# Performance work log

Measured on AMD Instinct MI355X. Metric: run time of the kernel, lower is better.

The kernel has to match this reference:

```python
import jax, jax.numpy as jnp
import numpy as np


def _conv1x1(x, W, b):
    # x: [B,C,H,W] (NCHW), W: [out,in] (1x1 conv kernel), b: [out]
    return jnp.einsum('bchw,oc->bohw', x, W) + b[None, :, None, None]


def setup_inputs() -> dict:
    key = jax.random.key(0)
    ks = jax.random.split(key, 12)
    B, C, H, W = 8, 256, 64, 64
    s = 1.0 / np.sqrt(C)
    x = jax.random.normal(ks[0], (B, C, H, W), dtype=jnp.float32)
    mask = jnp.round(jax.random.uniform(ks[1], (B, 1, H, W), dtype=jnp.float32))
    Wq = jax.random.normal(ks[2], (C, C), dtype=jnp.float32) * s
    bq = jax.random.normal(ks[3], (C,), dtype=jnp.float32) * 0.01
    Wk = jax.random.normal(ks[4], (C, C), dtype=jnp.float32) * s
    bk = jax.random.normal(ks[5], (C,), dtype=jnp.float32) * 0.01
    Wv = jax.random.normal(ks[6], (C, C), dtype=jnp.float32) * s
    bv = jax.random.normal(ks[7], (C,), dtype=jnp.float32) * 0.01
    Wo = jax.random.normal(ks[8], (C, C), dtype=jnp.float32) * s
    bo = jax.random.normal(ks[9], (C,), dtype=jnp.float32) * 0.01
    gamma = jnp.zeros((1,), dtype=jnp.float32)
    return {"input": x, "mask": mask, "Wq": Wq, "bq": bq, "Wk": Wk, "bk": bk,
            "Wv": Wv, "bv": bv, "Wo": Wo, "bo": bo, "gamma": gamma}


def reference(input, mask, Wq, bq, Wk, bk, Wv, bv, Wo, bo, gamma):
    B, C, H, W = input.shape
    # mask spatial size matches input -> no avg_pool branch (pre_feat is None)
    feat_f = input * mask            # foreground features -> queries
    feat_b = input * (1.0 - mask)    # background features -> keys/values
    q = _conv1x1(feat_f, Wq, bq).reshape(B, C, -1)   # [B,C,N]
    k = _conv1x1(feat_b, Wk, bk).reshape(B, C, -1)   # [B,C,N]
    v = _conv1x1(feat_b, Wv, bv).reshape(B, C, -1)   # [B,C,N]
    # scores[b,n,m] = q[:,n]^T k[:,m]  (no scaling, matching the torch code)
    scores = jnp.einsum('bcn,bcm->bnm', q, k)        # [B,N,N]
    attn = jax.nn.softmax(scores, axis=-1)
    out = jnp.einsum('bnm,bcm->bcn', attn, v).reshape(B, C, H, W)
    out = _conv1x1(out, Wo, bo)
    return out + gamma * input
```

## Files before the change

kernel.cpp:

```cpp
#include <hip/hip_runtime.h>

#define CC 256
#define NN 4096
#define NB 8
#define NM ((size_t)CC * NN)

typedef _Float16 f16;
typedef f16 f16x4 __attribute__((ext_vector_type(4)));
typedef f16 f16x8 __attribute__((ext_vector_type(8)));
typedef float f32x4 __attribute__((ext_vector_type(4)));
typedef unsigned int u32;

#define GLD16(gp, lp) __builtin_amdgcn_global_load_lds( \
    (const __attribute__((address_space(1))) u32*)(const void*)(gp), \
    (__attribute__((address_space(3))) u32*)(void*)(lp), 16, 0, 0)

__global__ __launch_bounds__(256) void mask_scan_kernel(
    const float* __restrict__ mask, int* __restrict__ posm, int* __restrict__ counts)
{
    const int b = blockIdx.x;
    const int t = threadIdx.x;
    const int lane = t & 63, w = t >> 6;
    __shared__ int wsum[4];
    const float* mp = mask + (size_t)b * NN;
    int* pp = posm + (size_t)b * NN;

    int loc[16], cnt = 0;
#pragma unroll
    for (int i = 0; i < 16; ++i) {
        loc[i] = cnt;
        cnt += (mp[t * 16 + i] == 0.0f) ? 1 : 0;
    }
    int inc = cnt;
#pragma unroll
    for (int d = 1; d < 64; d <<= 1) {
        int v = __shfl_up(inc, d, 64);
        if (lane >= d) inc += v;
    }
    if (lane == 63) wsum[w] = inc;
    int exc = inc - cnt;
    __syncthreads();
    int base = exc;
    for (int i = 0; i < w; ++i) base += wsum[i];
#pragma unroll
    for (int i = 0; i < 16; ++i)
        pp[t * 16 + i] = (mp[t * 16 + i] == 0.0f) ? (base + loc[i]) : -1;
    if (t == 0) counts[b] = wsum[0] + wsum[1] + wsum[2] + wsum[3];
}

__global__ __launch_bounds__(256, 2) void proj_fused_kernel(
    const float* __restrict__ x, const float* __restrict__ mask,
    const float* __restrict__ Wq, const float* __restrict__ bq,
    const float* __restrict__ Wk, const float* __restrict__ bk,
    const float* __restrict__ Wv, const float* __restrict__ bv,
    f16* __restrict__ wsh, const int* __restrict__ posm,
    const int* __restrict__ counts, int b0)
{
    __shared__ f16x8 xf[2048];
    __shared__ f16x8 xb[2048];

    const int t = threadIdx.x;
    const int lane = t & 63, w = t >> 6;
    const int l16 = lane & 15, quad = lane >> 4;
    const int slot = blockIdx.x;
    const int b = b0 + slot;
    const int n0 = blockIdx.y * 64;
    const float* xp = x + (size_t)b * NM;
    f16* base = wsh + (size_t)slot * 4 * NM;
    const int* pom = posm + (size_t)b * NN;

    float mf  = mask[(size_t)b * NN + n0 + lane];
    float mbk = 1.0f - mf;
#pragma unroll
    for (int i = 0; i < 8; ++i) {
        int cb = w * 8 + i;
        const float* col = xp + (size_t)cb * 8 * NN + n0 + lane;
        f16x8 vf, vb;
#pragma unroll
        for (int u = 0; u < 8; ++u) {
            float xv = col[(size_t)u * NN];
            vf[u] = (f16)(xv * mf);
            vb[u] = (f16)(xv * mbk);
        }
        int unit = ((cb >> 2) * 4 + (lane >> 4)) * 64 + (cb & 3) * 16 + (lane & 15);
        xf[unit] = vf;
        xb[unit] = vb;
    }
    __syncthreads();

#pragma unroll
    for (int pr = 0; pr < 6; ++pr) {
        int j0  = w * 12 + pr * 2;
        int p   = j0 >> 4;
        int oc0 = j0 & 15;
        const float* W    = (p == 0) ? Wq : (p == 1) ? Wk : Wv;
        const float* bias = (p == 0) ? bq : (p == 1) ? bk : bv;
        const f16x8* bt   = (p == 0) ? xf : xb;

        f16x8 wf[2][8];
#pragma unroll
        for (int h = 0; h < 2; ++h) {
            const float* wrow = W + (size_t)((oc0 + h) * 16 + l16) * CC + quad * 8;
#pragma unroll
            for (int kc = 0; kc < 8; ++kc) {
                float4 a = *(const float4*)(wrow + kc * 32);
                float4 c = *(const float4*)(wrow + kc * 32 + 4);
                f16x8 f;
                f[0] = (f16)a.x; f[1] = (f16)a.y; f[2] = (f16)a.z; f[3] = (f16)a.w;
                f[4] = (f16)c.x; f[5] = (f16)c.y; f[6] = (f16)c.z; f[7] = (f16)c.w;
                wf[h][kc] = f;
            }
        }
        f32x4 acc[2][4];
#pragma unroll
        for (int h = 0; h < 2; ++h)
#pragma unroll
            for (int nc = 0; nc < 4; ++nc) acc[h][nc] = (f32x4){0.f, 0.f, 0.f, 0.f};
#pragma unroll
        for (int nc = 0; nc < 4; ++nc)
#pragma unroll
            for (int kc = 0; kc < 8; ++kc) {
                f16x8 bf = bt[(kc * 4 + nc) * 64 + lane];
                acc[0][nc] = __builtin_amdgcn_mfma_f32_16x16x32_f16(wf[0][kc], bf, acc[0][nc], 0, 0, 0);
                acc[1][nc] = __builtin_amdgcn_mfma_f32_16x16x32_f16(wf[1][kc], bf, acc[1][nc], 0, 0, 0);
            }
#pragma unroll
        for (int h = 0; h < 2; ++h) {
            int oc = oc0 + h;
            float bvv[4];
#pragma unroll
            for (int r = 0; r < 4; ++r) bvv[r] = bias[oc * 16 + quad * 4 + r];
            if (p == 2) {
                f16* vpl = base + 2 * NM;
#pragma unroll
                for (int nc = 0; nc < 4; ++nc) {
                    int cp = pom[n0 + nc * 16 + l16];
                    if (cp >= 0) {
#pragma unroll
                        for (int r = 0; r < 4; ++r)
                            vpl[(size_t)(oc * 16 + quad * 4 + r) * NN + cp] =
                                (f16)(acc[h][nc][r] + bvv[r]);
                    }
                }
            } else if (p == 1) {
                f16* kpl = base + NM;
#pragma unroll
                for (int nc = 0; nc < 4; ++nc) {
                    int cp = pom[n0 + nc * 16 + l16];
                    if (cp >= 0) {
                        f16x4 pk;
#pragma unroll
                        for (int r = 0; r < 4; ++r) pk[r] = (f16)(acc[h][nc][r] + bvv[r]);
                        *(f16x4*)(kpl + (size_t)cp * CC + oc * 16 + quad * 4) = pk;
                    }
                }
            } else {
                f16* qpl = base;
#pragma unroll
                for (int nc = 0; nc < 4; ++nc) {
                    f16x4 pk;
#pragma unroll
                    for (int r = 0; r < 4; ++r) pk[r] = (f16)(acc[h][nc][r] + bvv[r]);
                    *(f16x4*)(qpl + (size_t)(n0 + nc * 16 + l16) * CC + oc * 16 + quad * 4) = pk;
                }
            }
        }
    }

    if (blockIdx.y == 0) {
        int Fb = counts[b];
        int Mp = (Fb + 31) & ~31;
        int pad = Mp - Fb;
        if (pad > 0) {
            f16* kpl = base + NM;
            f16* vpl = base + 2 * NM;
            f16x8 z8;
#pragma unroll
            for (int i = 0; i < 8; ++i) z8[i] = (f16)0.0f;
            for (int idx = t; idx < pad * 32; idx += 256)
                *(f16x8*)(kpl + (size_t)(Fb + idx / 32) * CC + (idx & 31) * 8) = z8;
            for (int idx = t; idx < pad * CC; idx += 256)
                vpl[(size_t)(idx / pad) * NN + Fb + (idx % pad)] = (f16)0.0f;
        }
    }
}

__global__ __launch_bounds__(256, 2) void flash_kernel(
    f16* __restrict__ wsh, const float* __restrict__ bk,
    const float* __restrict__ bv, const int* __restrict__ counts, int b0)
{
    __shared__ f16x8 klds[2][1024];
    __shared__ f16x8 vlds[2][1024];
    __shared__ f16 pbuf[4][16 * 40];

    const int t    = threadIdx.x;
    const int w    = t >> 6;
    const int lane = t & 63;
    const int l16  = lane & 15;
    const int quad = lane >> 4;
    const int slot = blockIdx.x;
    const int n0   = blockIdx.y * 64;

    f16* base = wsh + (size_t)slot * 4 * NM;
    const f16* qt = base;
    const f16* kt = base + NM;
    const f16* vp = base + 2 * NM;
    f16* op       = base + 3 * NM;

    const int Fb = counts[b0 + slot];
    const int nt = (Fb + 31) >> 5;

    int koff[4], voff[4];
#pragma unroll
    for (int i = 0; i < 4; ++i) {
        int u = i * 256 + t;
        koff[i] = (((u >> 9) & 1) * 16 + (u & 15)) * CC
                + ((u >> 6) & 7) * 32 + ((u >> 4) & 3) * 8;
        voff[i] = ((u >> 6) * 16 + (u & 15)) * NN + ((u >> 4) & 3) * 8;
    }

#define ISSUE(m0_, b_) do {                                                     \
    _Pragma("unroll")                                                           \
    for (int i_ = 0; i_ < 4; ++i_)                                              \
        GLD16(kt + (size_t)(m0_) * CC + koff[i_],                               \
              (f16*)&klds[b_][i_ * 256 + w * 64]);                              \
    _Pragma("unroll")                                                           \
    for (int i_ = 0; i_ < 4; ++i_)                                              \
        GLD16(vp + (size_t)(m0_) + voff[i_],                                    \
              (f16*)&vlds[b_][i_ * 256 + w * 64]);                              \
} while (0)

    const int nrow = n0 + w * 16 + l16;
    f16x8 qf[8];
#pragma unroll
    for (int kc = 0; kc < 8; ++kc)
        qf[kc] = *(const f16x8*)(qt + (size_t)nrow * CC + kc * 32 + quad * 8);
#pragma unroll
    for (int kc = 0; kc < 8; ++kc)
        asm volatile("" :: "v"(qf[kc]));
    asm volatile("s_waitcnt vmcnt(0)" ::: "memory");

    f32x4 oacc[17];
#pragma unroll
    for (int i = 0; i < 17; ++i) oacc[i] = (f32x4){0.f, 0.f, 0.f, 0.f};
    float M[4] = {-3.0e38f, -3.0e38f, -3.0e38f, -3.0e38f};

    f16* pw = &pbuf[w][0];
    f16x8 ones;
#pragma unroll
    for (int i = 0; i < 8; ++i) ones[i] = (f16)1.0f;

    if (nt > 0) ISSUE(0, 0);
    int cur = 0;

    for (int it = 0; it < nt; ++it) {
        if (it + 1 < nt) {
            ISSUE((it + 1) * 32, cur ^ 1);
            asm volatile("s_waitcnt vmcnt(8)" ::: "memory");
        } else {
            asm volatile("s_waitcnt vmcnt(0)" ::: "memory");
        }
        __builtin_amdgcn_s_barrier();
        asm volatile("" ::: "memory");

        f32x4 s[2];
        s[0] = (f32x4){0.f, 0.f, 0.f, 0.f};
        s[1] = (f32x4){0.f, 0.f, 0.f, 0.f};
        __builtin_amdgcn_s_setprio(1);
#pragma unroll
        for (int kc = 0; kc < 8; ++kc) {
            f16x8 k0 = klds[cur][kc * 64 + lane];
            f16x8 k1 = klds[cur][(8 + kc) * 64 + lane];
            s[0] = __builtin_amdgcn_mfma_f32_16x16x32_f16(qf[kc], k0, s[0], 0, 0, 0);
            s[1] = __builtin_amdgcn_mfma_f32_16x16x32_f16(qf[kc], k1, s[1], 0, 0, 0);
        }
        __builtin_amdgcn_s_setprio(0);

        if (((it + 1) << 5) > Fb) {
#pragma unroll
            for (int ms = 0; ms < 2; ++ms)
                if (it * 32 + ms * 16 + l16 >= Fb) {
#pragma unroll
                    for (int r = 0; r < 4; ++r) s[ms][r] = -3.0e38f;
                }
        }

        bool up = false;
#pragma unroll
        for (int ms = 0; ms < 2; ++ms)
#pragma unroll
            for (int r = 0; r < 4; ++r) up |= (s[ms][r] > M[r]);
        if (__any(up)) {
            float alpha[4];
#pragma unroll
            for (int r = 0; r < 4; ++r) {
                float tm = fmaxf(s[0][r], s[1][r]);
                tm = fmaxf(tm, __shfl_xor(tm, 1, 64));
                tm = fmaxf(tm, __shfl_xor(tm, 2, 64));
                tm = fmaxf(tm, __shfl_xor(tm, 4, 64));
                tm = fmaxf(tm, __shfl_xor(tm, 8, 64));
                float Mn = fmaxf(M[r], tm);
                alpha[r] = __expf(M[r] - Mn);
                M[r] = Mn;
            }
#pragma unroll
            for (int cs = 0; cs < 17; ++cs)
#pragma unroll
                for (int r = 0; r < 4; ++r) oacc[cs][r] *= alpha[r];
        }
#pragma unroll
        for (int ms = 0; ms < 2; ++ms)
#pragma unroll
            for (int r = 0; r < 4; ++r)
                pw[(quad * 4 + r) * 40 + ms * 16 + l16] = (f16)__expf(s[ms][r] - M[r]);
        asm volatile("s_waitcnt lgkmcnt(0)" ::: "memory");
        f16x8 pf = *(const f16x8*)(pw + l16 * 40 + quad * 8);

        __builtin_amdgcn_s_setprio(1);
#pragma unroll
        for (int cs = 0; cs < 16; ++cs) {
            f16x8 vf = vlds[cur][cs * 64 + lane];
            oacc[cs] = __builtin_amdgcn_mfma_f32_16x16x32_f16(pf, vf, oacc[cs], 0, 0, 0);
        }
        oacc[16] = __builtin_amdgcn_mfma_f32_16x16x32_f16(pf, ones, oacc[16], 0, 0, 0);
        __builtin_amdgcn_s_setprio(0);

        asm volatile("" ::: "memory");
        __builtin_amdgcn_s_barrier();
        cur ^= 1;
    }
    asm volatile("s_waitcnt vmcnt(0)" ::: "memory");

    {
        float cn = 0.f;
#pragma unroll
        for (int kc = 0; kc < 8; ++kc) {
            const float* bkp = bk + kc * 32 + quad * 8;
#pragma unroll
            for (int j = 0; j < 8; ++j)
                cn += (float)qf[kc][j] * bkp[j];
        }
        cn += __shfl_xor(cn, 16, 64);
        cn += __shfl_xor(cn, 32, 64);
        const float Ff = (float)(NN - Fb);
        float aw[4], wv[4];
#pragma unroll
        for (int r = 0; r < 4; ++r) {
            float cr = __shfl(cn, quad * 4 + r, 64);
            float Mn = fmaxf(M[r], cr);
            aw[r] = __expf(M[r] - Mn);
            wv[r] = Ff * __expf(cr - Mn);
            M[r] = Mn;
        }
#pragma unroll
        for (int cs = 0; cs < 16; ++cs) {
            float bvc = bv[cs * 16 + l16];
#pragma unroll
            for (int r = 0; r < 4; ++r)
                oacc[cs][r] = oacc[cs][r] * aw[r] + wv[r] * bvc;
        }
#pragma unroll
        for (int r = 0; r < 4; ++r)
            oacc[16][r] = oacc[16][r] * aw[r] + wv[r];
    }

    float inv[4];
#pragma unroll
    for (int r = 0; r < 4; ++r) inv[r] = 1.0f / oacc[16][r];
#pragma unroll
    for (int cs = 0; cs < 16; ++cs)
#pragma unroll
        for (int r = 0; r < 4; ++r)
            op[(size_t)(cs * 16 + l16) * NN + n0 + w * 16 + quad * 4 + r] =
                (f16)(oacc[cs][r] * inv[r]);
#undef ISSUE
}

__global__ __launch_bounds__(256, 2) void final_kernel(
    const f16* __restrict__ wsh, const float* __restrict__ Wo,
    const float* __restrict__ bo, const float* __restrict__ x,
    const float* __restrict__ gamma, float* __restrict__ outall, int b0)
{
    __shared__ f16x8 ot[2048];

    const int t = threadIdx.x;
    const int lane = t & 63, w = t >> 6;
    const int l16 = lane & 15, quad = lane >> 4;
    const int slot = blockIdx.x;
    const int b = b0 + slot;
    const int n0 = blockIdx.y * 64;
    const f16* O = wsh + ((size_t)slot * 4 + 3) * NM;
    const float* xp = x + (size_t)b * NM;
    float* outp = outall + (size_t)b * NM;

#pragma unroll
    for (int i = 0; i < 8; ++i) {
        int cb = w * 8 + i;
        const f16* col = O + (size_t)cb * 8 * NN + n0 + lane;
        f16x8 v;
#pragma unroll
        for (int u = 0; u < 8; ++u) v[u] = col[(size_t)u * NN];
        ot[((cb >> 2) * 4 + (lane >> 4)) * 64 + (cb & 3) * 16 + (lane & 15)] = v;
    }
    __syncthreads();

    float g = gamma[0];
#pragma unroll
    for (int pr = 0; pr < 2; ++pr) {
        int oc0 = w * 4 + pr * 2;
        f16x8 wf[2][8];
#pragma unroll
        for (int h = 0; h < 2; ++h) {
            const float* wrow = Wo + (size_t)((oc0 + h) * 16 + l16) * CC + quad * 8;
#pragma unroll
            for (int kc = 0; kc < 8; ++kc) {
                float4 a = *(const float4*)(wrow + kc * 32);
                float4 c = *(const float4*)(wrow + kc * 32 + 4);
                f16x8 f;
                f[0] = (f16)a.x; f[1] = (f16)a.y; f[2] = (f16)a.z; f[3] = (f16)a.w;
                f[4] = (f16)c.x; f[5] = (f16)c.y; f[6] = (f16)c.z; f[7] = (f16)c.w;
                wf[h][kc] = f;
            }
        }
        f32x4 acc[2][4];
#pragma unroll
        for (int h = 0; h < 2; ++h)
#pragma unroll
            for (int nc = 0; nc < 4; ++nc) acc[h][nc] = (f32x4){0.f, 0.f, 0.f, 0.f};
#pragma unroll
        for (int nc = 0; nc < 4; ++nc)
#pragma unroll
            for (int kc = 0; kc < 8; ++kc) {
                f16x8 bf = ot[(kc * 4 + nc) * 64 + lane];
                acc[0][nc] = __builtin_amdgcn_mfma_f32_16x16x32_f16(wf[0][kc], bf, acc[0][nc], 0, 0, 0);
                acc[1][nc] = __builtin_amdgcn_mfma_f32_16x16x32_f16(wf[1][kc], bf, acc[1][nc], 0, 0, 0);
            }
#pragma unroll
        for (int h = 0; h < 2; ++h) {
            int oc = oc0 + h;
            float bvv[4];
#pragma unroll
            for (int r = 0; r < 4; ++r) bvv[r] = bo[oc * 16 + quad * 4 + r];
#pragma unroll
            for (int nc = 0; nc < 4; ++nc)
#pragma unroll
                for (int r = 0; r < 4; ++r) {
                    size_t o = oc * 16 + quad * 4 + r;
                    size_t n = n0 + nc * 16 + l16;
                    outp[o * NN + n] = acc[h][nc][r] + bvv[r] + g * xp[o * NN + n];
                }
        }
    }
}

__global__ __launch_bounds__(256) void ones_kernel(float* __restrict__ out, int total)
{
    for (int i = blockIdx.x * 256 + threadIdx.x; i < total; i += gridDim.x * 256)
        out[i] = 1.0f;
}

extern "C" void kernel_launch(void* const* d_in, const int* in_sizes, int n_in,
                              void* d_out, int out_size, void* d_ws, size_t ws_size,
                              hipStream_t stream)
{
    const float* x     = (const float*)d_in[0];
    const float* mask  = (const float*)d_in[1];
    const float* Wq    = (const float*)d_in[2];
    const float* bq    = (const float*)d_in[3];
    const float* Wk    = (const float*)d_in[4];
    const float* bk    = (const float*)d_in[5];
    const float* Wv    = (const float*)d_in[6];
    const float* bv    = (const float*)d_in[7];
    const float* Wo    = (const float*)d_in[8];
    const float* bo    = (const float*)d_in[9];
    const float* gamma = (const float*)d_in[10];
    float* out = (float*)d_out;

    const size_t slot_bytes = 4 * NM * sizeof(f16);
    f16* wsh = (f16*)d_ws;
    int nb = (int)(ws_size / slot_bytes);
    if (nb < 1) {
        ones_kernel<<<2048, 256, 0, stream>>>(out, out_size);
        return;
    }
    if (nb > NB) nb = NB;

    int* scratch = (int*)out + ((size_t)out_size - (size_t)(NB * NN + 64));
    int* posm   = scratch;
    int* counts = scratch + NB * NN;
    mask_scan_kernel<<<NB, 256, 0, stream>>>(mask, posm, counts);

    for (int b0 = 0; b0 < NB; b0 += nb) {
        int nbc = NB - b0; if (nbc > nb) nbc = nb;
        dim3 gT(nbc, NN / 64);
        proj_fused_kernel<<<gT, 256, 0, stream>>>(x, mask, Wq, bq, Wk, bk, Wv, bv,
                                                  wsh, posm, counts, b0);
        flash_kernel<<<gT, 256, 0, stream>>>(wsh, bk, bv, counts, b0);
        final_kernel<<<gT, 256, 0, stream>>>(wsh, Wo, bo, x, gamma, out, b0);
    }
}
```

Baseline: 336.3 us.

## Process two query tiles per wave in flash kernel to reuse K/V loads

Each wave now handles 32 query rows (two 16-row halves) instead of 16, so every K and V fragment read from LDS feeds two MFMAs, and the grid has half as many blocks along N. This halves the K/V global-to-LDS traffic per query. The cost is roughly double the accumulator registers, with launch bounds lowered to one block per SM, which cuts occupancy and latency hiding. It also adds a lazy max-rescale threshold (rescale only when a score exceeds the running max by more than 8), which skips the rescale step more often but depends on fp16 headroom for exp values up to e^8.

```diff
diff --git a/kernel.cpp b/kernel.cpp
--- a/kernel.cpp
+++ b/kernel.cpp
@@ -185,13 +185,13 @@
     }
 }
 
-__global__ __launch_bounds__(256, 2) void flash_kernel(
+__global__ __launch_bounds__(256, 1) void flash_kernel(
     f16* __restrict__ wsh, const float* __restrict__ bk,
     const float* __restrict__ bv, const int* __restrict__ counts, int b0)
 {
     __shared__ f16x8 klds[2][1024];
     __shared__ f16x8 vlds[2][1024];
-    __shared__ f16 pbuf[4][16 * 40];
+    __shared__ f16 pbuf[4][32 * 40];
 
     const int t    = threadIdx.x;
     const int w    = t >> 6;
@@ -199,7 +199,7 @@
     const int l16  = lane & 15;
     const int quad = lane >> 4;
     const int slot = blockIdx.x;
-    const int n0   = blockIdx.y * 64;
+    const int n0   = blockIdx.y * 128;
 
     f16* base = wsh + (size_t)slot * 4 * NM;
     const f16* qt = base;
@@ -230,20 +230,31 @@
               (f16*)&vlds[b_][i_ * 256 + w * 64]);                              \
 } while (0)
 
-    const int nrow = n0 + w * 16 + l16;
-    f16x8 qf[8];
-#pragma unroll
-    for (int kc = 0; kc < 8; ++kc)
-        qf[kc] = *(const f16x8*)(qt + (size_t)nrow * CC + kc * 32 + quad * 8);
-#pragma unroll
-    for (int kc = 0; kc < 8; ++kc)
-        asm volatile("" :: "v"(qf[kc]));
+    f16x8 qf[2][8];
+#pragma unroll
+    for (int h = 0; h < 2; ++h) {
+        int nrow = n0 + w * 32 + h * 16 + l16;
+#pragma unroll
+        for (int kc = 0; kc < 8; ++kc)
+            qf[h][kc] = *(const f16x8*)(qt + (size_t)nrow * CC + kc * 32 + quad * 8);
+    }
+#pragma unroll
+    for (int h = 0; h < 2; ++h)
+#pragma unroll
+        for (int kc = 0; kc < 8; ++kc)
+            asm volatile("" :: "v"(qf[h][kc]));
     asm volatile("s_waitcnt vmcnt(0)" ::: "memory");
 
-    f32x4 oacc[17];
-#pragma unroll
-    for (int i = 0; i < 17; ++i) oacc[i] = (f32x4){0.f, 0.f, 0.f, 0.f};
-    float M[4] = {-3.0e38f, -3.0e38f, -3.0e38f, -3.0e38f};
+    f32x4 oacc[2][17];
+#pragma unroll
+    for (int h = 0; h < 2; ++h)
+#pragma unroll
+        for (int i = 0; i < 17; ++i) oacc[h][i] = (f32x4){0.f, 0.f, 0.f, 0.f};
+    float M[2][4];
+#pragma unroll
+    for (int h = 0; h < 2; ++h)
+#pragma unroll
+        for (int r = 0; r < 4; ++r) M[h][r] = -3.0e38f;
 
     f16* pw = &pbuf[w][0];
     f16x8 ones;
@@ -263,16 +274,20 @@
         __builtin_amdgcn_s_barrier();
         asm volatile("" ::: "memory");
 
-        f32x4 s[2];
-        s[0] = (f32x4){0.f, 0.f, 0.f, 0.f};
-        s[1] = (f32x4){0.f, 0.f, 0.f, 0.f};
+        f32x4 s[2][2];
+#pragma unroll
+        for (int h = 0; h < 2; ++h)
+#pragma unroll
+            for (int ms = 0; ms < 2; ++ms) s[h][ms] = (f32x4){0.f, 0.f, 0.f, 0.f};
         __builtin_amdgcn_s_setprio(1);
 #pragma unroll
         for (int kc = 0; kc < 8; ++kc) {
             f16x8 k0 = klds[cur][kc * 64 + lane];
             f16x8 k1 = klds[cur][(8 + kc) * 64 + lane];
-            s[0] = __builtin_amdgcn_mfma_f32_16x16x32_f16(qf[kc], k0, s[0], 0, 0, 0);
-            s[1] = __builtin_amdgcn_mfma_f32_16x16x32_f16(qf[kc], k1, s[1], 0, 0, 0);
+            s[0][0] = __builtin_amdgcn_mfma_f32_16x16x32_f16(qf[0][kc], k0, s[0][0], 0, 0, 0);
+            s[1][0] = __builtin_amdgcn_mfma_f32_16x16x32_f16(qf[1][kc], k0, s[1][0], 0, 0, 0);
+            s[0][1] = __builtin_amdgcn_mfma_f32_16x16x32_f16(qf[0][kc], k1, s[0][1], 0, 0, 0);
+            s[1][1] = __builtin_amdgcn_mfma_f32_16x16x32_f16(qf[1][kc], k1, s[1][1], 0, 0, 0);
         }
         __builtin_amdgcn_s_setprio(0);
 
@@ -281,48 +296,63 @@
             for (int ms = 0; ms < 2; ++ms)
                 if (it * 32 + ms * 16 + l16 >= Fb) {
 #pragma unroll
-                    for (int r = 0; r < 4; ++r) s[ms][r] = -3.0e38f;
+                    for (int h = 0; h < 2; ++h)
+#pragma unroll
+                        for (int r = 0; r < 4; ++r) s[h][ms][r] = -3.0e38f;
                 }
         }
 
         bool up = false;
 #pragma unroll
-        for (int ms = 0; ms < 2; ++ms)
-#pragma unroll
-            for (int r = 0; r < 4; ++r) up |= (s[ms][r] > M[r]);
+        for (int h = 0; h < 2; ++h)
+#pragma unroll
+            for (int ms = 0; ms < 2; ++ms)
+#pragma unroll
+                for (int r = 0; r < 4; ++r) up |= (s[h][ms][r] > M[h][r] + 8.0f);
         if (__any(up)) {
-            float alpha[4];
-#pragma unroll
-            for (int r = 0; r < 4; ++r) {
-                float tm = fmaxf(s[0][r], s[1][r]);
-                tm = fmaxf(tm, __shfl_xor(tm, 1, 64));
-                tm = fmaxf(tm, __shfl_xor(tm, 2, 64));
-                tm = fmaxf(tm, __shfl_xor(tm, 4, 64));
-                tm = fmaxf(tm, __shfl_xor(tm, 8, 64));
-                float Mn = fmaxf(M[r], tm);
-                alpha[r] = __expf(M[r] - Mn);
-                M[r] = Mn;
+#pragma unroll
+            for (int h = 0; h < 2; ++h) {
+                float alpha[4];
+#pragma unroll
+                for (int r = 0; r < 4; ++r) {
+                    float tm = fmaxf(s[h][0][r], s[h][1][r]);
+                    tm = fmaxf(tm, __shfl_xor(tm, 1, 64));
+                    tm = fmaxf(tm, __shfl_xor(tm, 2, 64));
+                    tm = fmaxf(tm, __shfl_xor(tm, 4, 64));
+                    tm = fmaxf(tm, __shfl_xor(tm, 8, 64));
+                    float Mn = fmaxf(M[h][r], tm);
+                    alpha[r] = __expf(M[h][r] - Mn);
+                    M[h][r] = Mn;
+                }
+#pragma unroll
+                for (int cs = 0; cs < 17; ++cs)
+#pragma unroll
+                    for (int r = 0; r < 4; ++r) oacc[h][cs][r] *= alpha[r];
             }
-#pragma unroll
-            for (int cs = 0; cs < 17; ++cs)
-#pragma unroll
-                for (int r = 0; r < 4; ++r) oacc[cs][r] *= alpha[r];
-        }
-#pragma unroll
-        for (int ms = 0; ms < 2; ++ms)
-#pragma unroll
-            for (int r = 0; r < 4; ++r)
-                pw[(quad * 4 + r) * 40 + ms * 16 + l16] = (f16)__expf(s[ms][r] - M[r]);
+        }
+#pragma unroll
+        for (int h = 0; h < 2; ++h)
+#pragma unroll
+            for (int ms = 0; ms < 2; ++ms)
+#pragma unroll
+                for (int r = 0; r < 4; ++r)
+                    pw[(h * 16 + quad * 4 + r) * 40 + ms * 16 + l16] =
+                        (f16)__expf(s[h][ms][r] - M[h][r]);
         asm volatile("s_waitcnt lgkmcnt(0)" ::: "memory");
-        f16x8 pf = *(const f16x8*)(pw + l16 * 40 + quad * 8);
+        f16x8 pf[2];
+#pragma unroll
+        for (int h = 0; h < 2; ++h)
+            pf[h] = *(const f16x8*)(pw + (h * 16 + l16) * 40 + quad * 8);
 
         __builtin_amdgcn_s_setprio(1);
 #pragma unroll
         for (int cs = 0; cs < 16; ++cs) {
             f16x8 vf = vlds[cur][cs * 64 + lane];
-            oacc[cs] = __builtin_amdgcn_mfma_f32_16x16x32_f16(pf, vf, oacc[cs], 0, 0, 0);
-        }
-        oacc[16] = __builtin_amdgcn_mfma_f32_16x16x32_f16(pf, ones, oacc[16], 0, 0, 0);
+            oacc[0][cs] = __builtin_amdgcn_mfma_f32_16x16x32_f16(pf[0], vf, oacc[0][cs], 0, 0, 0);
+            oacc[1][cs] = __builtin_amdgcn_mfma_f32_16x16x32_f16(pf[1], vf, oacc[1][cs], 0, 0, 0);
+        }
+        oacc[0][16] = __builtin_amdgcn_mfma_f32_16x16x32_f16(pf[0], ones, oacc[0][16], 0, 0, 0);
+        oacc[1][16] = __builtin_amdgcn_mfma_f32_16x16x32_f16(pf[1], ones, oacc[1][16], 0, 0, 0);
         __builtin_amdgcn_s_setprio(0);
 
         asm volatile("" ::: "memory");
@@ -331,48 +361,52 @@
     }
     asm volatile("s_waitcnt vmcnt(0)" ::: "memory");
 
-    {
+    const float Ff = (float)(NN - Fb);
+#pragma unroll
+    for (int h = 0; h < 2; ++h) {
         float cn = 0.f;
 #pragma unroll
         for (int kc = 0; kc < 8; ++kc) {
             const float* bkp = bk + kc * 32 + quad * 8;
 #pragma unroll
             for (int j = 0; j < 8; ++j)
-                cn += (float)qf[kc][j] * bkp[j];
+                cn += (float)qf[h][kc][j] * bkp[j];
         }
         cn += __shfl_xor(cn, 16, 64);
         cn += __shfl_xor(cn, 32, 64);
-        const float Ff = (float)(NN - Fb);
         float aw[4], wv[4];
 #pragma unroll
         for (int r = 0; r < 4; ++r) {
             float cr = __shfl(cn, quad * 4 + r, 64);
-            float Mn = fmaxf(M[r], cr);
-            aw[r] = __expf(M[r] - Mn);
+            float Mn = fmaxf(M[h][r], cr);
+            aw[r] = __expf(M[h][r] - Mn);
             wv[r] = Ff * __expf(cr - Mn);
-            M[r] = Mn;
+            M[h][r] = Mn;
         }
 #pragma unroll
         for (int cs = 0; cs < 16; ++cs) {
             float bvc = bv[cs * 16 + l16];
 #pragma unroll
             for (int r = 0; r < 4; ++r)
-                oacc[cs][r] = oacc[cs][r] * aw[r] + wv[r] * bvc;
+                oacc[h][cs][r] = oacc[h][cs][r] * aw[r] + wv[r] * bvc;
         }
 #pragma unroll
         for (int r = 0; r < 4; ++r)
-            oacc[16][r] = oacc[16][r] * aw[r] + wv[r];
-    }
-
-    float inv[4];
-#pragma unroll
-    for (int r = 0; r < 4; ++r) inv[r] = 1.0f / oacc[16][r];
-#pragma unroll
-    for (int cs = 0; cs < 16; ++cs)
-#pragma unroll
-        for (int r = 0; r < 4; ++r)
-            op[(size_t)(cs * 16 + l16) * NN + n0 + w * 16 + quad * 4 + r] =
-                (f16)(oacc[cs][r] * inv[r]);
+            oacc[h][16][r] = oacc[h][16][r] * aw[r] + wv[r];
+    }
+
+#pragma unroll
+    for (int h = 0; h < 2; ++h) {
+        float inv[4];
+#pragma unroll
+        for (int r = 0; r < 4; ++r) inv[r] = 1.0f / oacc[h][16][r];
+#pragma unroll
+        for (int cs = 0; cs < 16; ++cs)
+#pragma unroll
+            for (int r = 0; r < 4; ++r)
+                op[(size_t)(cs * 16 + l16) * NN + n0 + w * 32 + h * 16 + quad * 4 + r] =
+                    (f16)(oacc[h][cs][r] * inv[r]);
+    }
 #undef ISSUE
 }
 
@@ -493,9 +527,10 @@
     for (int b0 = 0; b0 < NB; b0 += nb) {
         int nbc = NB - b0; if (nbc > nb) nbc = nb;
         dim3 gT(nbc, NN / 64);
+        dim3 gF(nbc, NN / 128);
         proj_fused_kernel<<<gT, 256, 0, stream>>>(x, mask, Wq, bq, Wk, bk, Wv, bv,
                                                   wsh, posm, counts, b0);
-        flash_kernel<<<gT, 256, 0, stream>>>(wsh, bk, bv, counts, b0);
+        flash_kernel<<<gF, 256, 0, stream>>>(wsh, bk, bv, counts, b0);
         final_kernel<<<gT, 256, 0, stream>>>(wsh, Wo, bo, x, gamma, out, b0);
     }
 }
```

Result: slower. 413.8 us (+23.0%).
